# Optimization experiments

Hardware: AMD Instinct MI355X
Metric: run time of the kernel (lower is better)

The kernel has to match this reference:

```python
import jax, jax.numpy as jnp
import numpy as np

BATCH = 1024
N_KPS = 24
N_IN = 6
N_HID = 128
N_OUT = 2
N_EDGES = N_KPS * (N_KPS - 1)  # 552, fully-connected minus self-loops
BN_EPS = 1e-5


def _xavier(key, shape):
    # torch xavier_normal_: std = sqrt(2 / (fan_in + fan_out)); Linear weight is [out, in]
    std = np.sqrt(2.0 / (shape[0] + shape[1])).astype(np.float32)
    return jax.random.normal(key, shape, dtype=jnp.float32) * std


def _mlp(x, w1, b1, w2, b2, g, be):
    # Two-layer ELU MLP followed by training-mode BatchNorm1d over flattened (B*N, C)
    h = jax.nn.elu(jnp.einsum('bnd,hd->bnh', x, w1) + b1)
    h = jax.nn.elu(jnp.einsum('bnd,hd->bnh', h, w2) + b2)
    mean = h.mean(axis=(0, 1))
    var = h.var(axis=(0, 1))  # biased variance, as torch BN uses for normalization
    return g * (h - mean) * jax.lax.rsqrt(var + BN_EPS) + be


def setup_inputs() -> dict:
    key = jax.random.key(0)
    ks = jax.random.split(key, 12)
    # structural one-hot receiver/sender matrices for fully-connected graph (no self-loops)
    off = ~np.eye(N_KPS, dtype=bool)
    recv_idx, send_idx = np.nonzero(off)
    eye = np.eye(N_KPS, dtype=np.float32)
    rel_rec = jnp.asarray(eye[recv_idx])    # [E, N]
    rel_send = jnp.asarray(eye[send_idx])   # [E, N]

    inputs = jax.random.normal(ks[0], (BATCH, N_KPS, N_IN), dtype=jnp.float32)

    def mlp_params(k, n_in):
        k1, k2 = jax.random.split(k)
        return dict(
            w1=_xavier(k1, (N_HID, n_in)), b1=jnp.full((N_HID,), 0.1, jnp.float32),
            w2=_xavier(k2, (N_HID, N_HID)), b2=jnp.full((N_HID,), 0.1, jnp.float32),
            g=jnp.ones((N_HID,), jnp.float32), be=jnp.zeros((N_HID,), jnp.float32))

    m1 = mlp_params(ks[1], N_IN)
    m2 = mlp_params(ks[2], 2 * N_HID)
    m3 = mlp_params(ks[3], N_HID)
    m4 = mlp_params(ks[4], 3 * N_HID)
    fo_w = _xavier(ks[5], (N_OUT, N_HID * N_KPS))
    fo_b = jnp.full((N_OUT,), 0.1, jnp.float32)

    d = {'inputs': inputs, 'rel_rec': rel_rec, 'rel_send': rel_send,
         'fo_w': fo_w, 'fo_b': fo_b}
    for name, p in [('m1', m1), ('m2', m2), ('m3', m3), ('m4', m4)]:
        for k2, v in p.items():
            d[f'{name}_{k2}'] = v
    return d


def reference(inputs, rel_rec, rel_send,
              fo_w, fo_b,
              m1_w1, m1_b1, m1_w2, m1_b2, m1_g, m1_be,
              m2_w1, m2_b1, m2_w2, m2_b2, m2_g, m2_be,
              m3_w1, m3_b1, m3_w2, m3_b2, m3_g, m3_be,
              m4_w1, m4_b1, m4_w2, m4_b2, m4_g, m4_be):
    B, N = inputs.shape[0], inputs.shape[1]
    x = inputs.reshape(B, N, -1)

    def node2edge(x):  # [B,N,C] -> [B,E,2C]
        recv = jnp.einsum('en,bnc->bec', rel_rec, x)
        send = jnp.einsum('en,bnc->bec', rel_send, x)
        return jnp.concatenate([recv, send], axis=2)

    def edge2node(x):  # [B,E,C] -> [B,N,C], averaged by N (= incoming.size(1))
        return jnp.einsum('en,bec->bnc', rel_rec, x) / N

    x = _mlp(x, m1_w1, m1_b1, m1_w2, m1_b2, m1_g, m1_be)            # [B,N,H]
    x = _mlp(node2edge(x), m2_w1, m2_b1, m2_w2, m2_b2, m2_g, m2_be)  # [B,E,H]
    x_skip = x
    x = _mlp(edge2node(x), m3_w1, m3_b1, m3_w2, m3_b2, m3_g, m3_be)  # [B,N,H]
    x = node2edge(x)                                                  # [B,E,2H]
    x = jnp.concatenate([x, x_skip], axis=2)                          # [B,E,3H]
    x = _mlp(x, m4_w1, m4_b1, m4_w2, m4_b2, m4_g, m4_be)              # [B,E,H]
    x = edge2node(x)                                                  # [B,N,H]
    x = x.reshape(B, -1)                                              # [B,N*H]
    return x @ fo_w.T + fo_b                                          # [B,n_out]
```

## Files before the change

kernel.cpp:

```cpp
#include <hip/hip_runtime.h>

typedef __bf16 bf16;
typedef __bf16 b16x8 __attribute__((ext_vector_type(8)));
typedef __bf16 b16x4 __attribute__((ext_vector_type(4)));
typedef float f32x4 __attribute__((ext_vector_type(4)));

#define TB 256
#define LDA 136
#define NB 1024
#define NK 24
#define NE 552
#define NH 128
#define BEcnt (NB*NE)
#define BNODE (NB*NK)
#define EPS 1e-5f

#define S_BN1 0
#define S_BN3 256
#define S_SC2 512
#define S_SC4 768
#define S_B41 1024
#define WB_M1W2 0
#define WB_M2W1 16384
#define WB_M2W2 49152
#define WB_M3W1 65536
#define WB_M3W2 81920
#define WB_M4W1 98304
#define WB_M4W2 147456
#define WB_M4W1S 163840
#define OFF_WBF 8192ull
#define OFF_P2  368640ull
#define OFF_P4  (OFF_P2 + 6291456ull)
#define OFF_H1  (OFF_P4 + 6291456ull)
#define OFF_H3  (OFF_H1 + 6291456ull)
#define OFF_Y2R (OFF_H3 + 6291456ull)
#define OFF_Y2S (OFF_Y2R + 6291456ull)
#define OFF_Y4R (OFF_Y2S + 6291456ull)
#define OFF_Y4S (OFF_Y4R + 6291456ull)
#define OFF_Z2  (OFF_Y4S + 6291456ull)
#define OFF_Z4  (OFF_Z2  + 12582912ull)
#define OFF_H2  (OFF_Z4  + 12582912ull)

__device__ __forceinline__ float elu(float x){ return x > 0.f ? x : __expf(x) - 1.f; }

__device__ __forceinline__ void swizzle_bt(int id, int& b, int& tile4){
  int x = id & 7, j = id >> 3;
  int bt = j / 6;
  int tile = j - bt*6;
  b = x*128 + bt;
  tile4 = tile*4;
}

__device__ __forceinline__ void load_bfrags_bf(const bf16* W, int ldw, int k0,
                                               b16x8 bfr[4][2], int lane, int w){
  int n = lane & 15, q = lane >> 4;
  #pragma unroll
  for (int kb=0; kb<4; ++kb)
    #pragma unroll
    for (int t=0; t<2; ++t)
      bfr[kb][t] = *(const b16x8*)(W + (size_t)((w*2+t)*16 + n)*ldw + k0 + kb*32 + q*8);
}

__device__ __forceinline__ void gemm_regB(const bf16* As, const b16x8 bfr[4][2], f32x4 acc[6][2], int lane){
  int m = lane & 15, q = lane >> 4;
  #pragma unroll
  for (int kb=0; kb<4; ++kb){
    int ka = kb*32 + q*8;
    b16x8 a[6];
    #pragma unroll
    for (int mt=0; mt<6; ++mt)
      a[mt] = *(const b16x8*)(As + (mt*16+m)*LDA + ka);
    #pragma unroll
    for (int mt=0; mt<6; ++mt)
      #pragma unroll
      for (int t=0; t<2; ++t)
        acc[mt][t] = __builtin_amdgcn_mfma_f32_16x16x32_bf16(a[mt], bfr[kb][t], acc[mt][t], 0,0,0);
  }
}

__device__ __forceinline__ void zero_acc(f32x4 acc[6][2]){
  #pragma unroll
  for (int mt=0; mt<6; ++mt)
    #pragma unroll
    for (int t=0; t<2; ++t){ acc[mt][t][0]=0.f; acc[mt][t][1]=0.f; acc[mt][t][2]=0.f; acc[mt][t][3]=0.f; }
}

__device__ __forceinline__ void epilogue_to_lds(const f32x4 acc[6][2], const float* bias, bf16* As,
                                                int lane, int w, int validRows){
  int q = lane >> 4, n = lane & 15;
  #pragma unroll
  for (int mt=0; mt<6; ++mt)
    #pragma unroll
    for (int t=0; t<2; ++t){
      int col = (w*2+t)*16 + n;
      float bc = bias[col];
      #pragma unroll
      for (int i=0; i<4; ++i){
        int row = mt*16 + q*4 + i;
        float v = (row < validRows) ? elu(acc[mt][t][i] + bc) : 0.f;
        As[row*LDA + col] = (bf16)v;
      }
    }
}

__device__ __forceinline__ void write_acc_bf(const f32x4 acc[6][2], bf16* out, int lane, int w){
  int q = lane >> 4, n = lane & 15;
  #pragma unroll
  for (int mt=0; mt<6; ++mt)
    #pragma unroll
    for (int t=0; t<2; ++t){
      int col = (w*2+t)*16 + n;
      #pragma unroll
      for (int i=0; i<4; ++i)
        out[(size_t)(mt*16 + q*4 + i)*NH + col] = (bf16)acc[mt][t][i];
    }
}

__device__ __forceinline__ void store_and_stats(const bf16* As, bf16* g_out, float* statsDst,
                                                int tid, int validRows){
  for (int i = tid; i < validRows*16; i += TB){
    int row = i >> 4, c8 = (i & 15) << 3;
    *(b16x8*)(g_out + (size_t)row*NH + c8) = *(const b16x8*)(As + row*LDA + c8);
  }
  int c = tid & 127, half = tid >> 7;
  float s = 0.f, s2 = 0.f;
  for (int row = half; row < validRows; row += 2){
    float v = (float)As[row*LDA + c];
    s += v; s2 += v*v;
  }
  atomicAdd(&statsDst[c], s);
  atomicAdd(&statsDst[128+c], s2);
}

__device__ __forceinline__ void build_A_g(bf16* As, const bf16* yrG, const bf16* ysG,
                                          const float* bias, int tile4, int tid){
  for (int i=tid; i<96*16; i+=TB){
    int row = i >> 4, c8 = (i & 15) << 3;
    b16x8 o;
    if (row < 92){
      int rl = (row>=23)+(row>=46)+(row>=69);
      int j = row - rl*23;
      int s = j + (j >= tile4 + rl);
      b16x8 vr = *(const b16x8*)(yrG + (size_t)rl*NH + c8);
      b16x8 vs = *(const b16x8*)(ysG + (size_t)s*NH + c8);
      #pragma unroll
      for (int k=0; k<8; ++k) o[k] = (bf16)elu((float)vr[k] + (float)vs[k] + bias[c8+k]);
    } else {
      #pragma unroll
      for (int k=0; k<8; ++k) o[k] = (bf16)0.f;
    }
    *(b16x8*)(As + row*LDA + c8) = o;
  }
}

__device__ __forceinline__ void harvest_core(const f32x4 acc[6][2], const float* bias, bf16* As,
                                             float* zL, float* pL, int lane, int w){
  int q4 = (lane >> 4) << 2, n = lane & 15;
  int c0 = w*32 + n, c1 = c0 + 16;
  float b0 = bias[c0], b1 = bias[c1];
  float zs0[4] = {0,0,0,0}, zs1[4] = {0,0,0,0};
  float s0=0.f, p0=0.f, s1=0.f, p1=0.f;
  #pragma unroll
  for (int mt=0; mt<6; ++mt){
    #pragma unroll
    for (int i=0; i<4; ++i){
      const int R0 = mt*16 + i;
      int row = R0 + q4;
      bool ok = row < 92;
      float v0 = elu(acc[mt][0][i] + b0); v0 = ok ? v0 : 0.f;
      float v1 = elu(acc[mt][1][i] + b1); v1 = ok ? v1 : 0.f;
      if (As){
        As[row*LDA + c0] = (bf16)v0;
        As[row*LDA + c1] = (bf16)v1;
      }
      s0 += v0; p0 += v0*v0; s1 += v1; p1 += v1*v1;
      const int gLo = (R0>=23)+(R0>=46)+(R0>=69);
      const int gHi = ((R0+12)>=23)+((R0+12)>=46)+((R0+12)>=69);
      if (gLo == gHi){
        zs0[gLo] += v0; zs1[gLo] += v1;
      } else {
        const int bnd = (gHi==1) ? 23 : ((gHi==2) ? 46 : 69);
        bool hi = row >= bnd;
        zs0[gLo] += hi ? 0.f : v0;  zs0[gHi] += hi ? v0 : 0.f;
        zs1[gLo] += hi ? 0.f : v1;  zs1[gHi] += hi ? v1 : 0.f;
      }
    }
  }
  #pragma unroll
  for (int g=0; g<4; ++g){
    zs0[g] += __shfl_down(zs0[g],32); zs0[g] += __shfl_down(zs0[g],16);
    zs1[g] += __shfl_down(zs1[g],32); zs1[g] += __shfl_down(zs1[g],16);
  }
  s0 += __shfl_down(s0,32); s0 += __shfl_down(s0,16);
  p0 += __shfl_down(p0,32); p0 += __shfl_down(p0,16);
  s1 += __shfl_down(s1,32); s1 += __shfl_down(s1,16);
  p1 += __shfl_down(p1,32); p1 += __shfl_down(p1,16);
  if (lane < 16){
    #pragma unroll
    for (int g=0; g<4; ++g){
      zL[g*NH + c0] = zs0[g];
      zL[g*NH + c1] = zs1[g];
    }
    pL[c0] = s0; pL[128+c0] = p0;
    pL[c1] = s1; pL[128+c1] = p1;
  }
}

__global__ __launch_bounds__(TB) void k0_cvt(const float* __restrict__ s0, const float* __restrict__ s1,
    const float* __restrict__ s2, const float* __restrict__ s3, const float* __restrict__ s4,
    const float* __restrict__ s5, const float* __restrict__ s6, bf16* __restrict__ dst){
  int idx = (blockIdx.x*TB + threadIdx.x)*4;
  const float* sp; int base;
  if      (idx < 16384){ sp=s0; base=0; }
  else if (idx < 49152){ sp=s1; base=16384; }
  else if (idx < 65536){ sp=s2; base=49152; }
  else if (idx < 81920){ sp=s3; base=65536; }
  else if (idx < 98304){ sp=s4; base=81920; }
  else if (idx <147456){ sp=s5; base=98304; }
  else                 { sp=s6; base=147456; }
  f32x4 v = *(const f32x4*)(sp + (idx - base));
  b16x4 o; o[0]=(bf16)v[0]; o[1]=(bf16)v[1]; o[2]=(bf16)v[2]; o[3]=(bf16)v[3];
  *(b16x4*)(dst + idx) = o;
}

__global__ __launch_bounds__(TB) void k_fold41(const float* __restrict__ w41, const float* __restrict__ b41,
    const float* __restrict__ aff2, bf16* __restrict__ w41s, float* __restrict__ b41f){
  int tid = threadIdx.x;
  if (blockIdx.x < 16){
    int idx = (blockIdx.x*TB + tid)*4;
    int o = idx >> 7, k = idx & 127;
    f32x4 v = *(const f32x4*)(w41 + (size_t)o*384 + 256 + k);
    b16x4 r;
    #pragma unroll
    for (int j=0; j<4; ++j) r[j] = (bf16)(v[j] * aff2[k+j]);
    *(b16x4*)(w41s + idx) = r;
  } else if (tid < 128){
    const float* wr = w41 + (size_t)tid*384 + 256;
    float s = 0.f;
    for (int k=0; k<128; ++k) s += wr[k] * aff2[128+k];
    b41f[tid] = b41[tid] + s;
  }
}

__global__ __launch_bounds__(TB) void k1_mlp1(const float* __restrict__ in,
    const float* __restrict__ w1, const float* __restrict__ b1,
    const bf16* __restrict__ w2, const float* __restrict__ b2,
    bf16* __restrict__ h1, float* __restrict__ bn1){
  __shared__ alignas(16) bf16 As[96*LDA];
  __shared__ float w1s[128*6];
  __shared__ float b1s[128], b2s[128];
  __shared__ float ins[96*6];
  int tid = threadIdx.x;
  int row0 = blockIdx.x * 96;
  for (int i=tid; i<768; i+=TB) w1s[i] = w1[i];
  if (tid < 128){ b1s[tid]=b1[tid]; b2s[tid]=b2[tid]; }
  for (int i=tid; i<576; i+=TB) ins[i] = in[row0*6 + i];
  __syncthreads();
  for (int i=tid; i<96*32; i+=TB){
    int row = i >> 5, c4 = (i & 31) << 2;
    float x0=ins[row*6+0], x1=ins[row*6+1], x2=ins[row*6+2],
          x3=ins[row*6+3], x4=ins[row*6+4], x5=ins[row*6+5];
    #pragma unroll
    for (int j=0; j<4; ++j){
      int c = c4 + j;
      const float* wr = w1s + c*6;
      float s = b1s[c] + wr[0]*x0 + wr[1]*x1 + wr[2]*x2 + wr[3]*x3 + wr[4]*x4 + wr[5]*x5;
      As[row*LDA + c] = (bf16)elu(s);
    }
  }
  int lane = tid & 63, w = tid >> 6;
  b16x8 bfr[4][2];
  load_bfrags_bf(w2, 128, 0, bfr, lane, w);
  __syncthreads();
  f32x4 acc[6][2]; zero_acc(acc);
  gemm_regB(As, bfr, acc, lane);
  __syncthreads();
  epilogue_to_lds(acc, b2s, As, lane, w, 96);
  __syncthreads();
  store_and_stats(As, h1 + (size_t)row0*NH, bn1, tid, 96);
}

__global__ __launch_bounds__(TB) void k_project(const bf16* __restrict__ hin,
    const float* __restrict__ stats, float cnt,
    const float* __restrict__ g, const float* __restrict__ be,
    const bf16* __restrict__ Wp, int ldw,
    bf16* __restrict__ yr, bf16* __restrict__ ys){
  __shared__ alignas(16) bf16 As[96*LDA];
  __shared__ float scl[128], shf[128];
  int tid = threadIdx.x;
  int row0 = blockIdx.x * 96;
  if (tid < 128){
    float mean = stats[tid] / cnt;
    float var  = stats[128+tid] / cnt - mean*mean;
    float rs = rsqrtf(var + EPS);
    float sc = g[tid] * rs;
    scl[tid] = sc; shf[tid] = be[tid] - mean*sc;
  }
  __syncthreads();
  for (int i=tid; i<96*16; i+=TB){
    int row = i >> 4, c8 = (i & 15) << 3;
    b16x8 v = *(const b16x8*)(hin + (size_t)(row0+row)*NH + c8);
    b16x8 o;
    #pragma unroll
    for (int j=0; j<8; ++j) o[j] = (bf16)(scl[c8+j]*(float)v[j] + shf[c8+j]);
    *(b16x8*)(As + row*LDA + c8) = o;
  }
  int lane = tid & 63, w = tid >> 6;
  b16x8 bfr[4][2];
  load_bfrags_bf(Wp, ldw, 0, bfr, lane, w);
  __syncthreads();
  f32x4 acc[6][2]; zero_acc(acc);
  gemm_regB(As, bfr, acc, lane);
  write_acc_bf(acc, yr + (size_t)row0*NH, lane, w);
  load_bfrags_bf(Wp, ldw, 128, bfr, lane, w);
  zero_acc(acc);
  gemm_regB(As, bfr, acc, lane);
  write_acc_bf(acc, ys + (size_t)row0*NH, lane, w);
}

__global__ __launch_bounds__(TB,4) void k3_edge1(const bf16* __restrict__ y2r, const bf16* __restrict__ y2s,
    const float* __restrict__ b21, const bf16* __restrict__ w22, const float* __restrict__ b22,
    float* __restrict__ z2, float* __restrict__ P2, bf16* __restrict__ h2){
  __shared__ alignas(16) bf16 As[96*LDA];
  __shared__ float b1s[NH], b2s[NH];
  __shared__ float zL[512], pL[256];
  int tid = threadIdx.x;
  int b, tile4; swizzle_bt(blockIdx.x, b, tile4);
  if (tid < NH){ b1s[tid]=b21[tid]; b2s[tid]=b22[tid]; }
  int lane = tid & 63, w = tid >> 6;
  b16x8 bfr[4][2];
  load_bfrags_bf(w22, 128, 0, bfr, lane, w);
  __syncthreads();
  build_A_g(As, y2r + ((size_t)b*NK + tile4)*NH, y2s + (size_t)b*NK*NH, b1s, tile4, tid);
  __syncthreads();
  f32x4 acc[6][2]; zero_acc(acc);
  gemm_regB(As, bfr, acc, lane);
  __syncthreads();
  harvest_core(acc, b2s, As, zL, pL, lane, w);
  __syncthreads();
  float* zdst = z2 + (size_t)(b*NK + tile4)*NH;
  float* pdst = P2 + (size_t)blockIdx.x*256;
  if (tid < 128)      ((f32x4*)zdst)[tid]     = ((const f32x4*)zL)[tid];
  else if (tid < 192) ((f32x4*)pdst)[tid-128] = ((const f32x4*)pL)[tid-128];
  bf16* h2g = h2 + ((size_t)b*NE + tile4*23)*NH;
  for (int i=tid; i<92*16; i+=TB){
    int row = i >> 4, c8 = (i & 15) << 3;
    *(b16x8*)(h2g + (size_t)row*NH + c8) = *(const b16x8*)(As + row*LDA + c8);
  }
}

__global__ __launch_bounds__(TB) void k_bnred(const float* __restrict__ P,
    const float* __restrict__ g, const float* __restrict__ be, float* __restrict__ aff){
  __shared__ float rs[256], rq[256];
  int tid = threadIdx.x;
  int col = blockIdx.x*16 + (tid & 15);
  int chunk = tid >> 4;
  const float* p0 = P + (size_t)chunk*384*256 + col;
  float s=0.f, q=0.f;
  for (int r=0; r<384; ++r){
    s += p0[(size_t)r*256];
    q += p0[(size_t)r*256 + 128];
  }
  rs[tid]=s; rq[tid]=q;
  __syncthreads();
  if (tid < 16){
    float S=0.f, Q=0.f;
    #pragma unroll
    for (int c2=0; c2<16; ++c2){ S += rs[c2*16+tid]; Q += rq[c2*16+tid]; }
    int cc = blockIdx.x*16 + tid;
    float mean = S / (float)BEcnt;
    float var  = Q / (float)BEcnt - mean*mean;
    float sc = g[cc] * rsqrtf(var + EPS);
    aff[cc] = sc; aff[128+cc] = be[cc] - mean*sc;
  }
}

__global__ __launch_bounds__(TB) void k4a_mlp3(const float* __restrict__ z2,
    const float* __restrict__ aff2,
    const bf16* __restrict__ w31, const float* __restrict__ b31,
    const bf16* __restrict__ w32, const float* __restrict__ b32,
    bf16* __restrict__ h3, float* __restrict__ bn3){
  __shared__ alignas(16) bf16 As[96*LDA];
  __shared__ float scl[128], shf[128], b1s[128], b2s[128];
  int tid = threadIdx.x;
  int row0 = blockIdx.x * 96;
  if (tid < 128){
    scl[tid] = aff2[tid] * (1.f/24.f);
    shf[tid] = aff2[128+tid] * (23.f/24.f);
    b1s[tid] = b31[tid]; b2s[tid] = b32[tid];
  }
  __syncthreads();
  for (int i=tid; i<96*32; i+=TB){
    int rl = i >> 5, c4 = (i & 31) << 2;
    f32x4 v = *(const f32x4*)(z2 + (size_t)(row0+rl)*NH + c4);
    b16x4 o;
    #pragma unroll
    for (int k=0; k<4; ++k) o[k] = (bf16)(scl[c4+k]*v[k] + shf[c4+k]);
    *(b16x4*)(As + rl*LDA + c4) = o;
  }
  int lane = tid & 63, w = tid >> 6;
  b16x8 bfr[4][2];
  load_bfrags_bf(w31, 128, 0, bfr, lane, w);
  __syncthreads();
  f32x4 acc[6][2]; zero_acc(acc);
  gemm_regB(As, bfr, acc, lane);
  __syncthreads();
  epilogue_to_lds(acc, b1s, As, lane, w, 96);
  load_bfrags_bf(w32, 128, 0, bfr, lane, w);
  __syncthreads();
  zero_acc(acc);
  gemm_regB(As, bfr, acc, lane);
  __syncthreads();
  epilogue_to_lds(acc, b2s, As, lane, w, 96);
  __syncthreads();
  store_and_stats(As, h3 + (size_t)row0*NH, bn3, tid, 96);
}

__global__ __launch_bounds__(TB,3) void k5_edge2(
    const bf16* __restrict__ h2,
    const bf16* __restrict__ y4r, const bf16* __restrict__ y4s,
    const bf16* __restrict__ w41s, const float* __restrict__ b41f,
    const bf16* __restrict__ w42, const float* __restrict__ b42,
    float* __restrict__ z4, float* __restrict__ P4){
  __shared__ alignas(16) bf16 As[96*LDA];
  __shared__ alignas(16) bf16 yt4[28*LDA];
  __shared__ float b41s[NH], b42s[NH];
  __shared__ float zL[512], pL[256];
  int tid = threadIdx.x;
  int b, tile4; swizzle_bt(blockIdx.x, b, tile4);
  if (tid < NH){ b41s[tid]=b41f[tid]; b42s[tid]=b42[tid]; }
  int lane = tid & 63, w = tid >> 6;
  b16x8 bfr[4][2];
  load_bfrags_bf(w41s, 128, 0, bfr, lane, w);
  {
    const bf16* y4rG = y4r + ((size_t)b*NK + tile4)*NH;
    const bf16* y4sG = y4s + (size_t)b*NK*NH;
    for (int i=tid; i<448; i+=TB){
      int r = i >> 4, c8 = (i & 15) << 3;
      b16x8 v = (r < 4) ? *(const b16x8*)(y4rG + (size_t)r*NH + c8)
                        : *(const b16x8*)(y4sG + (size_t)(r-4)*NH + c8);
      *(b16x8*)(yt4 + r*LDA + c8) = v;
    }
  }
  {
    const bf16* h2g = h2 + ((size_t)b*NE + tile4*23)*NH;
    for (int i=tid; i<96*16; i+=TB){
      int row = i >> 4, c8 = (i & 15) << 3;
      b16x8 o;
      if (row < 92){
        o = *(const b16x8*)(h2g + (size_t)row*NH + c8);
      } else {
        #pragma unroll
        for (int j=0; j<8; ++j) o[j] = (bf16)0.f;
      }
      *(b16x8*)(As + row*LDA + c8) = o;
    }
  }
  __syncthreads();
  f32x4 acc[6][2]; zero_acc(acc);
  gemm_regB(As, bfr, acc, lane);
  load_bfrags_bf(w42, 128, 0, bfr, lane, w);
  __syncthreads();
  {
    int q = lane >> 4, n = lane & 15;
    #pragma unroll
    for (int mt=0; mt<6; ++mt)
      #pragma unroll
      for (int t=0; t<2; ++t){
        int col = w*32 + t*16 + n;
        #pragma unroll
        for (int i=0; i<4; ++i)
          As[(mt*16 + q*4 + i)*LDA + col] = (bf16)acc[mt][t][i];
      }
  }
  __syncthreads();
  for (int i=tid; i<96*16; i+=TB){
    int row = i >> 4, c8 = (i & 15) << 3;
    b16x8 o;
    if (row < 92){
      int rl = (row>=23)+(row>=46)+(row>=69);
      int j = row - rl*23;
      int s = j + (j >= tile4 + rl);
      b16x8 sk = *(const b16x8*)(As + row*LDA + c8);
      b16x8 vr = *(const b16x8*)(yt4 + rl*LDA + c8);
      b16x8 vs = *(const b16x8*)(yt4 + (4+s)*LDA + c8);
      #pragma unroll
      for (int k=0; k<8; ++k)
        o[k] = (bf16)elu((float)sk[k] + (float)vr[k] + (float)vs[k] + b41s[c8+k]);
    } else {
      #pragma unroll
      for (int k=0; k<8; ++k) o[k] = (bf16)0.f;
    }
    *(b16x8*)(As + row*LDA + c8) = o;
  }
  zero_acc(acc);
  __syncthreads();
  gemm_regB(As, bfr, acc, lane);
  harvest_core(acc, b42s, nullptr, zL, pL, lane, w);
  __syncthreads();
  float* zdst = z4 + (size_t)(b*NK + tile4)*NH;
  float* pdst = P4 + (size_t)blockIdx.x*256;
  if (tid < 128)      ((f32x4*)zdst)[tid]     = ((const f32x4*)zL)[tid];
  else if (tid < 192) ((f32x4*)pdst)[tid-128] = ((const f32x4*)pL)[tid-128];
}

__global__ __launch_bounds__(TB) void k6_out(const float* __restrict__ z4,
    const float* __restrict__ aff4,
    const float* __restrict__ fo_w, const float* __restrict__ fo_b, float* __restrict__ out){
  __shared__ float red[512];
  __shared__ float scl[128], shf[128];
  int tid = threadIdx.x, b = blockIdx.x;
  if (tid < 128){ scl[tid] = aff4[tid]; shf[tid] = aff4[128+tid]; }
  __syncthreads();
  const float inv24 = 1.f/24.f, f2324 = 23.f/24.f;
  float a0 = 0.f, a1 = 0.f;
  for (int i=tid; i<3072; i+=TB){
    int c = i & 127;
    float x = scl[c]*z4[(size_t)b*3072 + i]*inv24 + shf[c]*f2324;
    a0 += x * fo_w[i];
    a1 += x * fo_w[3072 + i];
  }
  red[tid] = a0; red[256+tid] = a1;
  __syncthreads();
  for (int st=128; st>0; st>>=1){
    if (tid < st){ red[tid] += red[tid+st]; red[256+tid] += red[256+tid+st]; }
    __syncthreads();
  }
  if (tid == 0){
    out[b*2+0] = red[0] + fo_b[0];
    out[b*2+1] = red[256] + fo_b[1];
  }
}

extern "C" void kernel_launch(void* const* d_in, const int* in_sizes, int n_in,
                              void* d_out, int out_size, void* d_ws, size_t ws_size,
                              hipStream_t stream){
  (void)in_sizes; (void)n_in; (void)out_size; (void)ws_size;
  const float* inputs = (const float*)d_in[0];
  const float* fo_w  = (const float*)d_in[3];
  const float* fo_b  = (const float*)d_in[4];
  const float* m1_w1=(const float*)d_in[5];  const float* m1_b1=(const float*)d_in[6];
  const float* m1_w2=(const float*)d_in[7];  const float* m1_b2=(const float*)d_in[8];
  const float* m1_g =(const float*)d_in[9];  const float* m1_be=(const float*)d_in[10];
  const float* m2_w1=(const float*)d_in[11]; const float* m2_b1=(const float*)d_in[12];
  const float* m2_w2=(const float*)d_in[13]; const float* m2_b2=(const float*)d_in[14];
  const float* m2_g =(const float*)d_in[15]; const float* m2_be=(const float*)d_in[16];
  const float* m3_w1=(const float*)d_in[17]; const float* m3_b1=(const float*)d_in[18];
  const float* m3_w2=(const float*)d_in[19]; const float* m3_b2=(const float*)d_in[20];
  const float* m3_g =(const float*)d_in[21]; const float* m3_be=(const float*)d_in[22];
  const float* m4_w1=(const float*)d_in[23]; const float* m4_b1=(const float*)d_in[24];
  const float* m4_w2=(const float*)d_in[25]; const float* m4_b2=(const float*)d_in[26];
  const float* m4_g =(const float*)d_in[27]; const float* m4_be=(const float*)d_in[28];

  char* ws = (char*)d_ws;
  float* stats = (float*)ws;
  bf16* wbf = (bf16*)(ws + OFF_WBF);
  float* P2 = (float*)(ws + OFF_P2);
  float* P4 = (float*)(ws + OFF_P4);
  bf16* h1  = (bf16*)(ws + OFF_H1);
  bf16* h3  = (bf16*)(ws + OFF_H3);
  bf16* y2r = (bf16*)(ws + OFF_Y2R);
  bf16* y2s = (bf16*)(ws + OFF_Y2S);
  bf16* y4r = (bf16*)(ws + OFF_Y4R);
  bf16* y4s = (bf16*)(ws + OFF_Y4S);
  float* z2  = (float*)(ws + OFF_Z2);
  float* z4  = (float*)(ws + OFF_Z4);
  bf16* h2  = (bf16*)(ws + OFF_H2);
  float* out = (float*)d_out;

  (void)hipMemsetAsync(d_ws, 0, 2048, stream);
  k0_cvt<<<160, TB, 0, stream>>>(m1_w2, m2_w1, m2_w2, m3_w1, m3_w2, m4_w1, m4_w2, wbf);
  k1_mlp1<<<256, TB, 0, stream>>>(inputs, m1_w1, m1_b1, wbf + WB_M1W2, m1_b2, h1, stats + S_BN1);
  k_project<<<256, TB, 0, stream>>>(h1, stats + S_BN1, (float)BNODE, m1_g, m1_be,
                                    wbf + WB_M2W1, 256, y2r, y2s);
  k3_edge1<<<6144, TB, 0, stream>>>(y2r, y2s, m2_b1, wbf + WB_M2W2, m2_b2, z2, P2, h2);
  k_bnred<<<8, TB, 0, stream>>>(P2, m2_g, m2_be, stats + S_SC2);
  k_fold41<<<17, TB, 0, stream>>>(m4_w1, m4_b1, stats + S_SC2, wbf + WB_M4W1S, stats + S_B41);
  k4a_mlp3<<<256, TB, 0, stream>>>(z2, stats + S_SC2, wbf + WB_M3W1, m3_b1,
                                   wbf + WB_M3W2, m3_b2, h3, stats + S_BN3);
  k_project<<<256, TB, 0, stream>>>(h3, stats + S_BN3, (float)BNODE, m3_g, m3_be,
                                    wbf + WB_M4W1, 384, y4r, y4s);
  k5_edge2<<<6144, TB, 0, stream>>>(h2, y4r, y4s,
                                    wbf + WB_M4W1S, stats + S_B41,
                                    wbf + WB_M4W2, m4_b2, z4, P4);
  k_bnred<<<8, TB, 0, stream>>>(P4, m4_g, m4_be, stats + S_SC4);
  k6_out<<<1024, TB, 0, stream>>>(z4, stats + S_SC4, fo_w, fo_b, out);
}
```

Measured before the change: 394.2 us.

## Replace per-block BN partials with bucketed atomics; shrink node-kernel tiles

Edge kernels stop writing per-block BN partial sums to a large global buffer. Instead they atomically accumulate into 64 bucketed stat slots, so the reduction kernel only sums 64 rows rather than 6144. The node-level kernels (mlp1, project, mlp3) drop from 96-row to 32-row tiles and launch three times as many blocks for better occupancy, with their BN stats spread over 8 atomic buckets. The memset grows to zero the larger stat area, and atomic contention on the buckets is the new cost.

```diff
diff --git a/kernel.cpp b/kernel.cpp
--- a/kernel.cpp
+++ b/kernel.cpp
@@ -16,10 +16,13 @@
 #define EPS 1e-5f
 
 #define S_BN1 0
-#define S_BN3 256
-#define S_SC2 512
-#define S_SC4 768
-#define S_B41 1024
+#define S_BN3 2048
+#define S_A2  4096
+#define S_A4  20480
+#define S_SC2 36864
+#define S_SC4 37120
+#define S_B41 37376
+#define STATS_ZERO_BYTES 147456
 #define WB_M1W2 0
 #define WB_M2W1 16384
 #define WB_M2W2 49152
@@ -28,10 +31,8 @@
 #define WB_M4W1 98304
 #define WB_M4W2 147456
 #define WB_M4W1S 163840
-#define OFF_WBF 8192ull
-#define OFF_P2  368640ull
-#define OFF_P4  (OFF_P2 + 6291456ull)
-#define OFF_H1  (OFF_P4 + 6291456ull)
+#define OFF_WBF 150528ull
+#define OFF_H1  516096ull
 #define OFF_H3  (OFF_H1 + 6291456ull)
 #define OFF_Y2R (OFF_H3 + 6291456ull)
 #define OFF_Y2S (OFF_Y2R + 6291456ull)
@@ -61,35 +62,39 @@
       bfr[kb][t] = *(const b16x8*)(W + (size_t)((w*2+t)*16 + n)*ldw + k0 + kb*32 + q*8);
 }
 
-__device__ __forceinline__ void gemm_regB(const bf16* As, const b16x8 bfr[4][2], f32x4 acc[6][2], int lane){
+template<int MT>
+__device__ __forceinline__ void gemm_regB_t(const bf16* As, const b16x8 bfr[4][2],
+                                            f32x4 acc[MT][2], int lane){
   int m = lane & 15, q = lane >> 4;
   #pragma unroll
   for (int kb=0; kb<4; ++kb){
     int ka = kb*32 + q*8;
-    b16x8 a[6];
-    #pragma unroll
-    for (int mt=0; mt<6; ++mt)
+    b16x8 a[MT];
+    #pragma unroll
+    for (int mt=0; mt<MT; ++mt)
       a[mt] = *(const b16x8*)(As + (mt*16+m)*LDA + ka);
     #pragma unroll
-    for (int mt=0; mt<6; ++mt)
+    for (int mt=0; mt<MT; ++mt)
       #pragma unroll
       for (int t=0; t<2; ++t)
         acc[mt][t] = __builtin_amdgcn_mfma_f32_16x16x32_bf16(a[mt], bfr[kb][t], acc[mt][t], 0,0,0);
   }
 }
 
-__device__ __forceinline__ void zero_acc(f32x4 acc[6][2]){
-  #pragma unroll
-  for (int mt=0; mt<6; ++mt)
+template<int MT>
+__device__ __forceinline__ void zero_acc_t(f32x4 acc[MT][2]){
+  #pragma unroll
+  for (int mt=0; mt<MT; ++mt)
     #pragma unroll
     for (int t=0; t<2; ++t){ acc[mt][t][0]=0.f; acc[mt][t][1]=0.f; acc[mt][t][2]=0.f; acc[mt][t][3]=0.f; }
 }
 
-__device__ __forceinline__ void epilogue_to_lds(const f32x4 acc[6][2], const float* bias, bf16* As,
-                                                int lane, int w, int validRows){
+template<int MT>
+__device__ __forceinline__ void epilogue_to_lds_t(const f32x4 acc[MT][2], const float* bias, bf16* As,
+                                                  int lane, int w, int validRows){
   int q = lane >> 4, n = lane & 15;
   #pragma unroll
-  for (int mt=0; mt<6; ++mt)
+  for (int mt=0; mt<MT; ++mt)
     #pragma unroll
     for (int t=0; t<2; ++t){
       int col = (w*2+t)*16 + n;
@@ -103,10 +108,11 @@
     }
 }
 
-__device__ __forceinline__ void write_acc_bf(const f32x4 acc[6][2], bf16* out, int lane, int w){
+template<int MT>
+__device__ __forceinline__ void write_acc_bf_t(const f32x4 acc[MT][2], bf16* out, int lane, int w){
   int q = lane >> 4, n = lane & 15;
   #pragma unroll
-  for (int mt=0; mt<6; ++mt)
+  for (int mt=0; mt<MT; ++mt)
     #pragma unroll
     for (int t=0; t<2; ++t){
       int col = (w*2+t)*16 + n;
@@ -116,20 +122,20 @@
     }
 }
 
-__device__ __forceinline__ void store_and_stats(const bf16* As, bf16* g_out, float* statsDst,
-                                                int tid, int validRows){
-  for (int i = tid; i < validRows*16; i += TB){
+__device__ __forceinline__ void store_and_stats32(const bf16* As, bf16* g_out, float* bucket,
+                                                  int tid){
+  for (int i = tid; i < 32*16; i += TB){
     int row = i >> 4, c8 = (i & 15) << 3;
     *(b16x8*)(g_out + (size_t)row*NH + c8) = *(const b16x8*)(As + row*LDA + c8);
   }
   int c = tid & 127, half = tid >> 7;
   float s = 0.f, s2 = 0.f;
-  for (int row = half; row < validRows; row += 2){
+  for (int row = half; row < 32; row += 2){
     float v = (float)As[row*LDA + c];
     s += v; s2 += v*v;
   }
-  atomicAdd(&statsDst[c], s);
-  atomicAdd(&statsDst[128+c], s2);
+  atomicAdd(&bucket[c], s);
+  atomicAdd(&bucket[128+c], s2);
 }
 
 __device__ __forceinline__ void build_A_g(bf16* As, const bf16* yrG, const bf16* ysG,
@@ -154,7 +160,7 @@
 }
 
 __device__ __forceinline__ void harvest_core(const f32x4 acc[6][2], const float* bias, bf16* As,
-                                             float* zL, float* pL, int lane, int w){
+                                             float* zL, float* sacc, int lane, int w){
   int q4 = (lane >> 4) << 2, n = lane & 15;
   int c0 = w*32 + n, c1 = c0 + 16;
   float b0 = bias[c0], b1 = bias[c1];
@@ -201,8 +207,8 @@
       zL[g*NH + c0] = zs0[g];
       zL[g*NH + c1] = zs1[g];
     }
-    pL[c0] = s0; pL[128+c0] = p0;
-    pL[c1] = s1; pL[128+c1] = p1;
+    atomicAdd(&sacc[c0], s0);     atomicAdd(&sacc[128+c0], p0);
+    atomicAdd(&sacc[c1], s1);     atomicAdd(&sacc[128+c1], p1);
   }
 }
 
@@ -246,17 +252,17 @@
     const float* __restrict__ w1, const float* __restrict__ b1,
     const bf16* __restrict__ w2, const float* __restrict__ b2,
     bf16* __restrict__ h1, float* __restrict__ bn1){
-  __shared__ alignas(16) bf16 As[96*LDA];
+  __shared__ alignas(16) bf16 As[32*LDA];
   __shared__ float w1s[128*6];
   __shared__ float b1s[128], b2s[128];
-  __shared__ float ins[96*6];
-  int tid = threadIdx.x;
-  int row0 = blockIdx.x * 96;
+  __shared__ float ins[32*6];
+  int tid = threadIdx.x;
+  int row0 = blockIdx.x * 32;
   for (int i=tid; i<768; i+=TB) w1s[i] = w1[i];
   if (tid < 128){ b1s[tid]=b1[tid]; b2s[tid]=b2[tid]; }
-  for (int i=tid; i<576; i+=TB) ins[i] = in[row0*6 + i];
-  __syncthreads();
-  for (int i=tid; i<96*32; i+=TB){
+  for (int i=tid; i<192; i+=TB) ins[i] = in[row0*6 + i];
+  __syncthreads();
+  for (int i=tid; i<32*32; i+=TB){
     int row = i >> 5, c4 = (i & 31) << 2;
     float x0=ins[row*6+0], x1=ins[row*6+1], x2=ins[row*6+2],
           x3=ins[row*6+3], x4=ins[row*6+4], x5=ins[row*6+5];
@@ -272,32 +278,35 @@
   b16x8 bfr[4][2];
   load_bfrags_bf(w2, 128, 0, bfr, lane, w);
   __syncthreads();
-  f32x4 acc[6][2]; zero_acc(acc);
-  gemm_regB(As, bfr, acc, lane);
-  __syncthreads();
-  epilogue_to_lds(acc, b2s, As, lane, w, 96);
-  __syncthreads();
-  store_and_stats(As, h1 + (size_t)row0*NH, bn1, tid, 96);
+  f32x4 acc[2][2]; zero_acc_t<2>(acc);
+  gemm_regB_t<2>(As, bfr, acc, lane);
+  __syncthreads();
+  epilogue_to_lds_t<2>(acc, b2s, As, lane, w, 32);
+  __syncthreads();
+  store_and_stats32(As, h1 + (size_t)row0*NH, bn1 + (blockIdx.x & 7)*256, tid);
 }
 
 __global__ __launch_bounds__(TB) void k_project(const bf16* __restrict__ hin,
-    const float* __restrict__ stats, float cnt,
+    const float* __restrict__ stats,
     const float* __restrict__ g, const float* __restrict__ be,
     const bf16* __restrict__ Wp, int ldw,
     bf16* __restrict__ yr, bf16* __restrict__ ys){
-  __shared__ alignas(16) bf16 As[96*LDA];
+  __shared__ alignas(16) bf16 As[32*LDA];
   __shared__ float scl[128], shf[128];
   int tid = threadIdx.x;
-  int row0 = blockIdx.x * 96;
+  int row0 = blockIdx.x * 32;
   if (tid < 128){
-    float mean = stats[tid] / cnt;
-    float var  = stats[128+tid] / cnt - mean*mean;
+    float s = 0.f, q2 = 0.f;
+    #pragma unroll
+    for (int k=0; k<8; ++k){ s += stats[k*256+tid]; q2 += stats[k*256+128+tid]; }
+    float mean = s / (float)BNODE;
+    float var  = q2 / (float)BNODE - mean*mean;
     float rs = rsqrtf(var + EPS);
     float sc = g[tid] * rs;
     scl[tid] = sc; shf[tid] = be[tid] - mean*sc;
   }
   __syncthreads();
-  for (int i=tid; i<96*16; i+=TB){
+  for (int i=tid; i<32*16; i+=TB){
     int row = i >> 4, c8 = (i & 15) << 3;
     b16x8 v = *(const b16x8*)(hin + (size_t)(row0+row)*NH + c8);
     b16x8 o;
@@ -309,21 +318,21 @@
   b16x8 bfr[4][2];
   load_bfrags_bf(Wp, ldw, 0, bfr, lane, w);
   __syncthreads();
-  f32x4 acc[6][2]; zero_acc(acc);
-  gemm_regB(As, bfr, acc, lane);
-  write_acc_bf(acc, yr + (size_t)row0*NH, lane, w);
+  f32x4 acc[2][2]; zero_acc_t<2>(acc);
+  gemm_regB_t<2>(As, bfr, acc, lane);
+  write_acc_bf_t<2>(acc, yr + (size_t)row0*NH, lane, w);
   load_bfrags_bf(Wp, ldw, 128, bfr, lane, w);
-  zero_acc(acc);
-  gemm_regB(As, bfr, acc, lane);
-  write_acc_bf(acc, ys + (size_t)row0*NH, lane, w);
+  zero_acc_t<2>(acc);
+  gemm_regB_t<2>(As, bfr, acc, lane);
+  write_acc_bf_t<2>(acc, ys + (size_t)row0*NH, lane, w);
 }
 
 __global__ __launch_bounds__(TB,4) void k3_edge1(const bf16* __restrict__ y2r, const bf16* __restrict__ y2s,
     const float* __restrict__ b21, const bf16* __restrict__ w22, const float* __restrict__ b22,
-    float* __restrict__ z2, float* __restrict__ P2, bf16* __restrict__ h2){
+    float* __restrict__ z2, float* __restrict__ acc2, bf16* __restrict__ h2){
   __shared__ alignas(16) bf16 As[96*LDA];
   __shared__ float b1s[NH], b2s[NH];
-  __shared__ float zL[512], pL[256];
+  __shared__ float zL[512];
   int tid = threadIdx.x;
   int b, tile4; swizzle_bt(blockIdx.x, b, tile4);
   if (tid < NH){ b1s[tid]=b21[tid]; b2s[tid]=b22[tid]; }
@@ -333,15 +342,13 @@
   __syncthreads();
   build_A_g(As, y2r + ((size_t)b*NK + tile4)*NH, y2s + (size_t)b*NK*NH, b1s, tile4, tid);
   __syncthreads();
-  f32x4 acc[6][2]; zero_acc(acc);
-  gemm_regB(As, bfr, acc, lane);
-  __syncthreads();
-  harvest_core(acc, b2s, As, zL, pL, lane, w);
+  f32x4 acc[6][2]; zero_acc_t<6>(acc);
+  gemm_regB_t<6>(As, bfr, acc, lane);
+  __syncthreads();
+  harvest_core(acc, b2s, As, zL, acc2 + (blockIdx.x & 63)*256, lane, w);
   __syncthreads();
   float* zdst = z2 + (size_t)(b*NK + tile4)*NH;
-  float* pdst = P2 + (size_t)blockIdx.x*256;
-  if (tid < 128)      ((f32x4*)zdst)[tid]     = ((const f32x4*)zL)[tid];
-  else if (tid < 192) ((f32x4*)pdst)[tid-128] = ((const f32x4*)pL)[tid-128];
+  if (tid < 128) ((f32x4*)zdst)[tid] = ((const f32x4*)zL)[tid];
   bf16* h2g = h2 + ((size_t)b*NE + tile4*23)*NH;
   for (int i=tid; i<92*16; i+=TB){
     int row = i >> 4, c8 = (i & 15) << 3;
@@ -349,17 +356,17 @@
   }
 }
 
-__global__ __launch_bounds__(TB) void k_bnred(const float* __restrict__ P,
+__global__ __launch_bounds__(TB) void k_bnred(const float* __restrict__ A,
     const float* __restrict__ g, const float* __restrict__ be, float* __restrict__ aff){
   __shared__ float rs[256], rq[256];
   int tid = threadIdx.x;
   int col = blockIdx.x*16 + (tid & 15);
   int chunk = tid >> 4;
-  const float* p0 = P + (size_t)chunk*384*256 + col;
   float s=0.f, q=0.f;
-  for (int r=0; r<384; ++r){
-    s += p0[(size_t)r*256];
-    q += p0[(size_t)r*256 + 128];
+  for (int r=0; r<4; ++r){
+    int row = chunk*4 + r;
+    s += A[row*256 + col];
+    q += A[row*256 + 128 + col];
   }
   rs[tid]=s; rq[tid]=q;
   __syncthreads();
@@ -380,17 +387,17 @@
     const bf16* __restrict__ w31, const float* __restrict__ b31,
     const bf16* __restrict__ w32, const float* __restrict__ b32,
     bf16* __restrict__ h3, float* __restrict__ bn3){
-  __shared__ alignas(16) bf16 As[96*LDA];
+  __shared__ alignas(16) bf16 As[32*LDA];
   __shared__ float scl[128], shf[128], b1s[128], b2s[128];
   int tid = threadIdx.x;
-  int row0 = blockIdx.x * 96;
+  int row0 = blockIdx.x * 32;
   if (tid < 128){
     scl[tid] = aff2[tid] * (1.f/24.f);
     shf[tid] = aff2[128+tid] * (23.f/24.f);
     b1s[tid] = b31[tid]; b2s[tid] = b32[tid];
   }
   __syncthreads();
-  for (int i=tid; i<96*32; i+=TB){
+  for (int i=tid; i<32*32; i+=TB){
     int rl = i >> 5, c4 = (i & 31) << 2;
     f32x4 v = *(const f32x4*)(z2 + (size_t)(row0+rl)*NH + c4);
     b16x4 o;
@@ -402,18 +409,18 @@
   b16x8 bfr[4][2];
   load_bfrags_bf(w31, 128, 0, bfr, lane, w);
   __syncthreads();
-  f32x4 acc[6][2]; zero_acc(acc);
-  gemm_regB(As, bfr, acc, lane);
-  __syncthreads();
-  epilogue_to_lds(acc, b1s, As, lane, w, 96);
+  f32x4 acc[2][2]; zero_acc_t<2>(acc);
+  gemm_regB_t<2>(As, bfr, acc, lane);
+  __syncthreads();
+  epilogue_to_lds_t<2>(acc, b1s, As, lane, w, 32);
   load_bfrags_bf(w32, 128, 0, bfr, lane, w);
   __syncthreads();
-  zero_acc(acc);
-  gemm_regB(As, bfr, acc, lane);
-  __syncthreads();
-  epilogue_to_lds(acc, b2s, As, lane, w, 96);
-  __syncthreads();
-  store_and_stats(As, h3 + (size_t)row0*NH, bn3, tid, 96);
+  zero_acc_t<2>(acc);
+  gemm_regB_t<2>(As, bfr, acc, lane);
+  __syncthreads();
+  epilogue_to_lds_t<2>(acc, b2s, As, lane, w, 32);
+  __syncthreads();
+  store_and_stats32(As, h3 + (size_t)row0*NH, bn3 + (blockIdx.x & 7)*256, tid);
 }
 
 __global__ __launch_bounds__(TB,3) void k5_edge2(
@@ -421,11 +428,11 @@
     const bf16* __restrict__ y4r, const bf16* __restrict__ y4s,
     const bf16* __restrict__ w41s, const float* __restrict__ b41f,
     const bf16* __restrict__ w42, const float* __restrict__ b42,
-    float* __restrict__ z4, float* __restrict__ P4){
+    float* __restrict__ z4, float* __restrict__ acc4){
   __shared__ alignas(16) bf16 As[96*LDA];
   __shared__ alignas(16) bf16 yt4[28*LDA];
   __shared__ float b41s[NH], b42s[NH];
-  __shared__ float zL[512], pL[256];
+  __shared__ float zL[512];
   int tid = threadIdx.x;
   int b, tile4; swizzle_bt(blockIdx.x, b, tile4);
   if (tid < NH){ b41s[tid]=b41f[tid]; b42s[tid]=b42[tid]; }
@@ -457,8 +464,8 @@
     }
   }
   __syncthreads();
-  f32x4 acc[6][2]; zero_acc(acc);
-  gemm_regB(As, bfr, acc, lane);
+  f32x4 acc[6][2]; zero_acc_t<6>(acc);
+  gemm_regB_t<6>(As, bfr, acc, lane);
   load_bfrags_bf(w42, 128, 0, bfr, lane, w);
   __syncthreads();
   {
@@ -493,15 +500,13 @@
     }
     *(b16x8*)(As + row*LDA + c8) = o;
   }
-  zero_acc(acc);
-  __syncthreads();
-  gemm_regB(As, bfr, acc, lane);
-  harvest_core(acc, b42s, nullptr, zL, pL, lane, w);
+  zero_acc_t<6>(acc);
+  __syncthreads();
+  gemm_regB_t<6>(As, bfr, acc, lane);
+  harvest_core(acc, b42s, nullptr, zL, acc4 + (blockIdx.x & 63)*256, lane, w);
   __syncthreads();
   float* zdst = z4 + (size_t)(b*NK + tile4)*NH;
-  float* pdst = P4 + (size_t)blockIdx.x*256;
-  if (tid < 128)      ((f32x4*)zdst)[tid]     = ((const f32x4*)zL)[tid];
-  else if (tid < 192) ((f32x4*)pdst)[tid-128] = ((const f32x4*)pL)[tid-128];
+  if (tid < 128) ((f32x4*)zdst)[tid] = ((const f32x4*)zL)[tid];
 }
 
 __global__ __launch_bounds__(TB) void k6_out(const float* __restrict__ z4,
@@ -555,8 +560,6 @@
   char* ws = (char*)d_ws;
   float* stats = (float*)ws;
   bf16* wbf = (bf16*)(ws + OFF_WBF);
-  float* P2 = (float*)(ws + OFF_P2);
-  float* P4 = (float*)(ws + OFF_P4);
   bf16* h1  = (bf16*)(ws + OFF_H1);
   bf16* h3  = (bf16*)(ws + OFF_H3);
   bf16* y2r = (bf16*)(ws + OFF_Y2R);
@@ -568,21 +571,22 @@
   bf16* h2  = (bf16*)(ws + OFF_H2);
   float* out = (float*)d_out;
 
-  (void)hipMemsetAsync(d_ws, 0, 2048, stream);
+  (void)hipMemsetAsync(d_ws, 0, STATS_ZERO_BYTES, stream);
   k0_cvt<<<160, TB, 0, stream>>>(m1_w2, m2_w1, m2_w2, m3_w1, m3_w2, m4_w1, m4_w2, wbf);
-  k1_mlp1<<<256, TB, 0, stream>>>(inputs, m1_w1, m1_b1, wbf + WB_M1W2, m1_b2, h1, stats + S_BN1);
-  k_project<<<256, TB, 0, stream>>>(h1, stats + S_BN1, (float)BNODE, m1_g, m1_be,
+  k1_mlp1<<<768, TB, 0, stream>>>(inputs, m1_w1, m1_b1, wbf + WB_M1W2, m1_b2, h1, stats + S_BN1);
+  k_project<<<768, TB, 0, stream>>>(h1, stats + S_BN1, m1_g, m1_be,
                                     wbf + WB_M2W1, 256, y2r, y2s);
-  k3_edge1<<<6144, TB, 0, stream>>>(y2r, y2s, m2_b1, wbf + WB_M2W2, m2_b2, z2, P2, h2);
-  k_bnred<<<8, TB, 0, stream>>>(P2, m2_g, m2_be, stats + S_SC2);
+  k3_edge1<<<6144, TB, 0, stream>>>(y2r, y2s, m2_b1, wbf + WB_M2W2, m2_b2, z2,
+                                    stats + S_A2, h2);
+  k_bnred<<<8, TB, 0, stream>>>(stats + S_A2, m2_g, m2_be, stats + S_SC2);
   k_fold41<<<17, TB, 0, stream>>>(m4_w1, m4_b1, stats + S_SC2, wbf + WB_M4W1S, stats + S_B41);
-  k4a_mlp3<<<256, TB, 0, stream>>>(z2, stats + S_SC2, wbf + WB_M3W1, m3_b1,
+  k4a_mlp3<<<768, TB, 0, stream>>>(z2, stats + S_SC2, wbf + WB_M3W1, m3_b1,
                                    wbf + WB_M3W2, m3_b2, h3, stats + S_BN3);
-  k_project<<<256, TB, 0, stream>>>(h3, stats + S_BN3, (float)BNODE, m3_g, m3_be,
+  k_project<<<768, TB, 0, stream>>>(h3, stats + S_BN3, m3_g, m3_be,
                                     wbf + WB_M4W1, 384, y4r, y4s);
   k5_edge2<<<6144, TB, 0, stream>>>(h2, y4r, y4s,
                                     wbf + WB_M4W1S, stats + S_B41,
-                                    wbf + WB_M4W2, m4_b2, z4, P4);
-  k_bnred<<<8, TB, 0, stream>>>(P4, m4_g, m4_be, stats + S_SC4);
+                                    wbf + WB_M4W2, m4_b2, z4, stats + S_A4);
+  k_bnred<<<8, TB, 0, stream>>>(stats + S_A4, m4_g, m4_be, stats + S_SC4);
   k6_out<<<1024, TB, 0, stream>>>(z4, stats + S_SC4, fo_w, fo_b, out);
 }
```

New measurement: 334.2 us. 15.2% less time.
